# Optimization experiments

Measured on AMD Instinct MI355X. Metric: run time of the kernel, lower is better.

Reference implementation:

```python
import jax, jax.numpy as jnp
import numpy as np

V, H, B, T, L, G = 32000, 256, 16, 128, 50, 8
BETA, GAMMA = 5.0, 2.0
ATOL = 1e-8  # torch.allclose(x, zeros) default atol (rtol term vanishes vs zero)


def setup_inputs() -> dict:
    key = jax.random.key(0)
    ks = jax.random.split(key, 17)
    u = 1.0 / np.sqrt(H)
    def U(k, shape):
        return jax.random.uniform(k, shape, jnp.float32, -u, u)
    return dict(
        recipe=jax.random.randint(ks[0], (B, T), 0, V),
        g=jax.random.randint(ks[1], (B, G), 0, V),
        ingr=jax.random.randint(ks[2], (B, L), 0, V),
        wv=jax.random.normal(ks[3], (V, H), jnp.float32) * 0.1,  # frozen word vectors
        w_ih=U(ks[4], (5 * H, H)),
        w_hh=U(ks[5], (5 * H, H)),
        b_ih=U(ks[6], (5 * H,)),
        b_hh=U(ks[7], (5 * H,)),
        Z=U(ks[8], (H, H)),
        Y=U(ks[9], (H, H)),
        U_g=U(ks[10], (H, H)),
        z_bias=U(ks[11], (H,)),
        y_bias=U(ks[12], (H,)),
        S=U(ks[13], (3, H)),
        P=U(ks[14], (H, H)),
        fcW=U(ks[15], (V, H)),
        fcb=U(ks[16], (V,)),
    )


def _cgru_forward(x, g_vec, E, w_ih, w_hh, b_ih, b_hh, Z, Y, U_g, z_bias, y_bias, S, P):
    # x: (B,T,H) batch_first; g_vec: (B,H); E: (B,L,H)
    ht0 = g_vec @ U_g.T                      # init_hidden
    a0 = jnp.zeros((x.shape[0], E.shape[1]), x.dtype)
    E0 = E                                   # (1-a)*E with a=0
    ot0 = jnp.zeros_like(x[:, 0])
    goal_term = g_vec @ Y.T + y_bias         # constant across steps

    def step(carry, x_t):
        ht, ot, a, E_new = carry
        is_zero = jnp.all(jnp.abs(x_t) <= ATOL)
        # --- cell ---
        gi = x_t @ w_ih.T + b_ih
        gh = ht @ w_hh.T + b_hh
        i_r, i_u, i_n, i_g, i_i = jnp.split(gi, 5, axis=1)
        h_r, h_u, h_n, h_g, h_i = jnp.split(gh, 5, axis=1)
        z_t = jax.nn.sigmoid(i_u + h_u)
        r_t = jax.nn.sigmoid(i_r + h_r)
        s_t = jax.nn.sigmoid(i_g + h_g)
        q_t = jax.nn.sigmoid(i_i + h_i)
        tmp = E_new.sum(axis=1)              # 'mlk -> mk'
        h_tilde = jnp.tanh(i_n + r_t * h_n + s_t * goal_term + q_t * (tmp @ Z.T + z_bias))
        ht2 = h_tilde + z_t * (ht - h_tilde)
        # --- attention read/write ---
        ref = jax.nn.softmax((BETA * ht2) @ S.T, axis=-1)   # (B,3)
        h_proj = ht2 @ P.T
        En = (1.0 - a)[:, :, None] * E
        alpha_n = jax.nn.softmax(GAMMA * jnp.einsum('mk,mlk->ml', h_proj, En), axis=-1)
        c_n = jnp.einsum('mlk,ml->mk', E, alpha_n)
        Eu = a[:, :, None] * E
        alpha_u = jax.nn.softmax(GAMMA * jnp.einsum('mk,mlk->ml', h_proj, Eu), axis=-1)
        c_u = jnp.einsum('mlk,ml->mk', E, alpha_u)
        out = ref[:, 0:1] * h_proj + ref[:, 1:2] * c_n + ref[:, 2:3] * c_u
        a2 = a + ref[:, 1:2] * alpha_n
        # skip update when input step is all-zero (faithful to torch.allclose guard)
        ht_o = jnp.where(is_zero, ht, ht2)
        ot_o = jnp.where(is_zero, ot, out)
        a_o = jnp.where(is_zero, a, a2)
        E_o = jnp.where(is_zero, E_new, En)
        return (ht_o, ot_o, a_o, E_o), ot_o

    (ht, ot, a, E_new), outs = jax.lax.scan(step, (ht0, ot0, a0, E0),
                                            jnp.transpose(x, (1, 0, 2)))
    output = jnp.transpose(outs, (1, 0, 2))  # back to batch_first (B,T,H)
    return output, ht, a, E_new


def reference(recipe, g, ingr, wv, w_ih, w_hh, b_ih, b_hh, Z, Y, U_g,
              z_bias, y_bias, S, P, fcW, fcb):
    recipe_embed = wv[recipe]           # (B,T,H)
    goal_embed = wv[g].sum(axis=1)      # (B,H)
    E = wv[ingr]                        # (B,L,H)
    output, ht, a, E_new = _cgru_forward(recipe_embed, goal_embed, E,
                                         w_ih, w_hh, b_ih, b_hh, Z, Y, U_g,
                                         z_bias, y_bias, S, P)
    logits = output @ fcW.T + fcb       # (B,T,V)
    return logits, ht, a, E_new
```

## Files before the change

### kernel.cpp

```cpp
#include <hip/hip_runtime.h>

#define Hd   256
#define Bd   16
#define Td   128
#define Ld   50
#define Vd   32000
#define G5H  1280

typedef __attribute__((ext_vector_type(8))) short short8v;
typedef __attribute__((ext_vector_type(4))) float f32x4;

__device__ __forceinline__ unsigned short f2bu(float f) {
  unsigned u = __float_as_uint(f);
  unsigned r = (u + 0x7fffu + ((u >> 16) & 1u)) >> 16;
  return (unsigned short)r;
}
__device__ __forceinline__ float bu2f(unsigned short b) {
  return __uint_as_float(((unsigned)b) << 16);
}
__device__ __forceinline__ float sigm(float x) { return 1.f / (1.f + __expf(-x)); }

__device__ __forceinline__ void st_devu(unsigned* p, unsigned v) {
  __hip_atomic_store(p, v, __ATOMIC_RELAXED, __HIP_MEMORY_SCOPE_AGENT);
}
__device__ __forceinline__ unsigned ld_devu(const unsigned* p) {
  return __hip_atomic_load((unsigned*)p, __ATOMIC_RELAXED, __HIP_MEMORY_SCOPE_AGENT);
}
__device__ __forceinline__ void st_devd(double* p, double v) {
  __hip_atomic_store(p, v, __ATOMIC_RELAXED, __HIP_MEMORY_SCOPE_AGENT);
}
__device__ __forceinline__ double ld_devd(const double* p) {
  return __hip_atomic_load((double*)p, __ATOMIC_RELAXED, __HIP_MEMORY_SCOPE_AGENT);
}
__device__ __forceinline__ double pk2(float a, float b) {
  union { double d; float2 f; } u; u.f = make_float2(a, b); return u.d;
}

__global__ __launch_bounds__(256) void conv_kernel(
    const float* __restrict__ wv, const float* __restrict__ w_ih,
    const float* __restrict__ fcW, const float* __restrict__ w_hh,
    const float* __restrict__ Zm, const float* __restrict__ Pm,
    unsigned short* __restrict__ wv_b, unsigned short* __restrict__ wih_b,
    unsigned short* __restrict__ fcw_b, unsigned short* __restrict__ whh_f,
    unsigned short* __restrict__ z_f, unsigned short* __restrict__ p_f)
{
  const long N0 = 2048000, N1 = N0 + 81920, N2 = N1 + 2048000;
  const long NW = 81920, NZ = 16384, NP = 16384;
  const long N5 = N2 + NW + NZ + NP;
  for (long idx = (long)blockIdx.x * blockDim.x + threadIdx.x; idx < N5;
       idx += (long)gridDim.x * blockDim.x) {
    if (idx < N2) {
      const float* src; unsigned short* dst; long off;
      if      (idx < N0) { src = wv;   dst = wv_b;  off = idx; }
      else if (idx < N1) { src = w_ih; dst = wih_b; off = idx - N0; }
      else               { src = fcW;  dst = fcw_b; off = idx - N1; }
      float4 v = *(const float4*)(src + off * 4);
      ushort4 o;
      o.x = f2bu(v.x); o.y = f2bu(v.y); o.z = f2bu(v.z); o.w = f2bu(v.w);
      *(ushort4*)(dst + off * 4) = o;
    } else {
      long u = idx - N2;
      const float* src; unsigned short* dst;
      if      (u < NW)      { src = w_hh; dst = whh_f; }
      else if (u < NW + NZ) { src = Zm;   dst = z_f;  u -= NW; }
      else                  { src = Pm;   dst = p_f;  u -= NW + NZ; }
      long frag = u >> 7;
      int g128 = (int)(u & 127);
      int lane = g128 >> 1, e0 = (g128 & 1) * 4;
      long T = frag >> 3; int ks = (int)(frag & 7);
      int lr = lane & 15, lg = lane >> 4;
      float4 v = *(const float4*)(src + (T * 16 + lr) * 256 + ks * 32 + lg * 8 + e0);
      ushort4 o;
      o.x = f2bu(v.x); o.y = f2bu(v.y); o.z = f2bu(v.z); o.w = f2bu(v.w);
      *(ushort4*)(dst + u * 4) = o;
    }
  }
}

__global__ __launch_bounds__(256) void prep_kernel(
    const int* __restrict__ g, const int* __restrict__ ingr,
    const float* __restrict__ wv, const float* __restrict__ Ug,
    const float* __restrict__ Ym, const float* __restrict__ yb,
    float* __restrict__ E_ws, float* __restrict__ sumE,
    float* __restrict__ goal_ws, float* __restrict__ HT0)
{
  __shared__ float ge[256];
  const int b = blockIdx.x, tid = threadIdx.x;
  float s = 0.f;
  for (int i = 0; i < 8; ++i) s += wv[((size_t)g[(b << 3) + i] << 8) + tid];
  ge[tid] = s;
  __syncthreads();
  float h0 = 0.f, gt = 0.f;
  const float* ur = Ug + (tid << 8);
  const float* yr = Ym + (tid << 8);
#pragma unroll 8
  for (int k = 0; k < Hd; k += 4) {
    float4 gv = *(const float4*)(ge + k);
    float4 uv = *(const float4*)(ur + k);
    float4 yv = *(const float4*)(yr + k);
    h0 = fmaf(gv.x, uv.x, h0); h0 = fmaf(gv.y, uv.y, h0);
    h0 = fmaf(gv.z, uv.z, h0); h0 = fmaf(gv.w, uv.w, h0);
    gt = fmaf(gv.x, yv.x, gt); gt = fmaf(gv.y, yv.y, gt);
    gt = fmaf(gv.z, yv.z, gt); gt = fmaf(gv.w, yv.w, gt);
  }
  HT0[(b << 8) + tid] = h0;
  goal_ws[(b << 8) + tid] = gt + yb[tid];
  float se = 0.f;
  for (int l = 0; l < Ld; ++l) {
    float v = wv[((size_t)ingr[b * Ld + l] << 8) + tid];
    E_ws[((size_t)(b * Ld + l) << 8) + tid] = v;
    se += v;
  }
  sumE[(b << 8) + tid] = se;
}

template <int MODE>
__global__ __launch_bounds__(256) void gemm_bf16(
    const unsigned short* __restrict__ A, const unsigned short* __restrict__ Bmat,
    const int* __restrict__ ridx, const float* __restrict__ bias,
    float* __restrict__ C)
{
  __shared__ unsigned short As[128 * 64];
  __shared__ unsigned short Bs[128 * 64];
  const int tid = threadIdx.x;
  const int m0 = blockIdx.x << 7, n0 = blockIdx.y << 7;
  const int wave = tid >> 6, lane = tid & 63;
  const int wm = wave >> 1, wn = wave & 1;
  const int lr = lane & 15, lg = lane >> 4;

  f32x4 acc[4][4];
#pragma unroll
  for (int i = 0; i < 4; ++i)
#pragma unroll
    for (int jj = 0; jj < 4; ++jj) acc[i][jj] = (f32x4){0.f, 0.f, 0.f, 0.f};

  const int srow = tid >> 1, shalf = tid & 1;
  const unsigned short* arow;
  {
    int gm = m0 + srow;
    if (MODE == 0) {
      int tt = gm >> 4, bb = gm & 15;
      arow = A + (size_t)ridx[bb * Td + tt] * Hd;
    } else {
      arow = A + (size_t)gm * Hd;
    }
  }
  const unsigned short* brow = Bmat + (size_t)(n0 + srow) * Hd;

  for (int k0 = 0; k0 < Hd; k0 += 64) {
#pragma unroll
    for (int c = 0; c < 4; ++c) {
      int k = shalf * 32 + c * 8;
      uint4 va = *(const uint4*)(arow + k0 + k);
      uint4 vb = *(const uint4*)(brow + k0 + k);
      int byo = (srow << 7) + ((k << 1) ^ ((srow & 7) << 4));
      *(uint4*)((char*)As + byo) = va;
      *(uint4*)((char*)Bs + byo) = vb;
    }
    __syncthreads();
#pragma unroll
    for (int kk = 0; kk < 2; ++kk) {
      short8v af[4], bfr[4];
      const int kb = kk * 32 + lg * 8;
#pragma unroll
      for (int i = 0; i < 4; ++i) {
        int ar = wm * 64 + i * 16 + lr;
        af[i] = *(const short8v*)((const char*)As + (ar << 7) + ((kb << 1) ^ ((ar & 7) << 4)));
        int br = wn * 64 + i * 16 + lr;
        bfr[i] = *(const short8v*)((const char*)Bs + (br << 7) + ((kb << 1) ^ ((br & 7) << 4)));
      }
#pragma unroll
      for (int i = 0; i < 4; ++i)
#pragma unroll
        for (int jj = 0; jj < 4; ++jj)
          acc[i][jj] = __builtin_amdgcn_mfma_f32_16x16x32_bf16(af[i], bfr[jj], acc[i][jj], 0, 0, 0);
    }
    __syncthreads();
  }
#pragma unroll
  for (int i = 0; i < 4; ++i)
#pragma unroll
    for (int jj = 0; jj < 4; ++jj) {
      int col = n0 + wn * 64 + jj * 16 + lr;
      float bv = bias[col];
#pragma unroll
      for (int r = 0; r < 4; ++r) {
        int row = m0 + wm * 64 + i * 16 + lg * 4 + r;
        float v = acc[i][jj][r] + bv;
        if (MODE == 0) {
          int tt = row >> 4, bb = row & 15;
          C[((size_t)(bb * Td + tt)) * G5H + col] = v;
        } else {
          C[(size_t)row * Vd + col] = v;
        }
      }
    }
}

#define RNN_SMEM 150080
__global__ __launch_bounds__(512, 1) void rnn_kernel(
    const unsigned short* __restrict__ whh_f, const unsigned short* __restrict__ z_f,
    const unsigned short* __restrict__ p_f, const float* __restrict__ b_hh,
    const float* __restrict__ Sm, const float* __restrict__ z_bias,
    const float* __restrict__ gi, const float* __restrict__ goal_ws,
    const float* __restrict__ E_ws, const float* __restrict__ sumE,
    const float* __restrict__ HT0,
    unsigned short* __restrict__ out_all, float* __restrict__ d_out,
    double* __restrict__ XH, double* __restrict__ XP, unsigned* __restrict__ FL)
{
  extern __shared__ char smem[];
  unsigned short* w_lds = (unsigned short*)(smem);
  unsigned short* z_lds = (unsigned short*)(smem + 81920);
  unsigned short* p_lds = (unsigned short*)(smem + 98304);
  unsigned short* E_lds = (unsigned short*)(smem + 114688);
  float* hp    = (float*)(smem + 141088);
  float* gh_l  = (float*)(smem + 142112);
  float* zd    = (float*)(smem + 142752);
  float* se    = (float*)(smem + 142880);
  float* gl    = (float*)(smem + 143904);
  float* bh    = (float*)(smem + 144032);
  float* zb    = (float*)(smem + 144672);
  float* Sl    = (float*)(smem + 144800);
  float* a_l   = (float*)(smem + 145184);
  float* d_l   = (float*)(smem + 145440);
  float* an_l  = (float*)(smem + 145696);
  float* au_l  = (float*)(smem + 145952);
  float* sd    = (float*)(smem + 146208);
  float* refl  = (float*)(smem + 146224);
  unsigned short* tp_hi = (unsigned short*)(smem + 146240);
  unsigned short* tp_lo = (unsigned short*)(smem + 146752);
  unsigned short* hs_hi = (unsigned short*)(smem + 147264);
  unsigned short* hs_lo = (unsigned short*)(smem + 147328);
  float* hrow  = (float*)(smem + 147392);
  unsigned short* ht_hi = (unsigned short*)(smem + 148416);
  unsigned short* ht_lo = (unsigned short*)(smem + 148928);
  float* gi_l  = (float*)(smem + 149440);

  const int b  = blockIdx.x >> 3;
  const int j  = blockIdx.x & 7;
  const int hc0 = j << 5;
  const int tid = threadIdx.x;
  const int lane = tid & 63, wid = tid >> 6;
  const int lr = lane & 15, lg = lane >> 4;
  unsigned* FLb = FL + (b << 5);

  for (int idx = tid; idx < 5120; idx += 512) {
    int f = idx >> 6, e = idx & 63;
    int q = f >> 3, ks = f & 7;
    int T = (q >> 1) * 16 + 2 * j + (q & 1);
    *(uint4*)(w_lds + ((size_t)f << 9) + e * 8) =
        *(const uint4*)(whh_f + (((size_t)T * 8 + ks) << 9) + e * 8);
  }
  for (int idx = tid; idx < 1024; idx += 512) {
    int f = idx >> 6, e = idx & 63;
    int T = 2 * j + (f >> 3), ks = f & 7;
    *(uint4*)(z_lds + ((size_t)f << 9) + e * 8) =
        *(const uint4*)(z_f + (((size_t)T * 8 + ks) << 9) + e * 8);
  }
  for (int idx = tid; idx < 1024; idx += 512) {
    int f = idx >> 6, e = idx & 63;
    *(uint4*)(p_lds + ((size_t)f << 9) + e * 8) =
        *(const uint4*)(p_f + (((size_t)f * 8 + j) << 9) + e * 8);
  }
  for (int idx = tid; idx < Ld * 256; idx += 512) {
    int l = idx >> 8, k = idx & 255;
    E_lds[l * 264 + (k >> 5) * 33 + (k & 31)] =
        f2bu(E_ws[((size_t)(b * Ld + l) << 8) + k]);
  }
  if (tid < 160) bh[tid] = b_hh[((tid >> 5) << 8) + hc0 + (tid & 31)];
  if (tid < 96) Sl[tid] = Sm[((tid >> 5) << 8) + hc0 + (tid & 31)];
  if (tid < 32) {
    gl[tid] = goal_ws[(b << 8) + hc0 + tid];
    zb[tid] = z_bias[hc0 + tid];
  }
  if (tid < 256) {
    float s0 = sumE[(b << 8) + tid];
    se[tid] = s0;
    unsigned short hi = f2bu(s0);
    tp_hi[tid] = hi; tp_lo[tid] = f2bu(s0 - bu2f(hi));
    float h0 = HT0[(b << 8) + tid];
    hrow[tid] = h0;
    unsigned short hh = f2bu(h0);
    ht_hi[tid] = hh; ht_lo[tid] = f2bu(h0 - bu2f(hh));
  }
  if (tid < 64) a_l[tid] = 0.f;
  __syncthreads();

  if (wid < 4) {
#pragma unroll
    for (int i = 0; i < 3; ++i) {
      int q = wid + 4 * i;
      if (q < 10) {
        f32x4 acc = (f32x4){0.f, 0.f, 0.f, 0.f};
#pragma unroll
        for (int ks = 0; ks < 8; ++ks) {
          short8v av = *(const short8v*)(w_lds + ((size_t)(q * 8 + ks) << 9) + (lane << 3));
          short8v bv = (short8v){0,0,0,0,0,0,0,0};
          if (lr < 2)
            bv = *(const short8v*)((lr == 0 ? ht_hi : ht_lo) + ks * 32 + (lg << 3));
          acc = __builtin_amdgcn_mfma_f32_16x16x32_bf16(av, bv, acc, 0, 0, 0);
        }
#pragma unroll
        for (int r = 0; r < 4; ++r) {
          float v = acc[r] + __shfl_xor(acc[r], 1);
          if (lr == 0) gh_l[q * 16 + lg * 4 + r] = v;
        }
      }
    }
  } else if (wid == 4 || wid == 5) {
    int tz = wid - 4;
    f32x4 acc = (f32x4){0.f, 0.f, 0.f, 0.f};
#pragma unroll
    for (int ks = 0; ks < 8; ++ks) {
      short8v av = *(const short8v*)(z_lds + ((size_t)(tz * 8 + ks) << 9) + (lane << 3));
      short8v bv = (short8v){0,0,0,0,0,0,0,0};
      if (lr < 2)
        bv = *(const short8v*)((lr == 0 ? tp_hi : tp_lo) + ks * 32 + (lg << 3));
      acc = __builtin_amdgcn_mfma_f32_16x16x32_bf16(av, bv, acc, 0, 0, 0);
    }
#pragma unroll
    for (int r = 0; r < 4; ++r) {
      float v = acc[r] + __shfl_xor(acc[r], 1);
      if (lr == 0) zd[tz * 16 + lg * 4 + r] = v;
    }
  }
  __syncthreads();
  {
    double* XHp = XH + ((size_t)((0 * 16 + b) * 8 + j)) * 16;
    double* XPp = XP + ((size_t)((0 * 16 + b) * 8 + j)) * 132;
    if (tid < 32) {
      int cl = tid;
      const float* gib = gi + ((size_t)(b * Td)) * G5H + hc0 + cl;
      float g_ir = gib[0], g_iu = gib[256], g_in = gib[512];
      float g_ig = gib[768], g_ii = gib[1024];
      float hr = gh_l[cl]       + bh[cl];
      float hu = gh_l[32 + cl]  + bh[32 + cl];
      float hn = gh_l[64 + cl]  + bh[64 + cl];
      float hg = gh_l[96 + cl]  + bh[96 + cl];
      float hq = gh_l[128 + cl] + bh[128 + cl];
      float rt = sigm(g_ir + hr), zt = sigm(g_iu + hu);
      float st = sigm(g_ig + hg), qt = sigm(g_ii + hq);
      float htl = tanhf(g_in + rt * hn + st * gl[cl] + qt * (zd[cl] + zb[cl]));
      float h2 = htl + zt * (hrow[hc0 + cl] - htl);
      unsigned short hi = f2bu(h2);
      hs_hi[cl] = hi; hs_lo[cl] = f2bu(h2 - bu2f(hi));
      float h2o = __shfl_xor(h2, 1);
      if (!(cl & 1)) st_devd(XHp + (cl >> 1), pk2(h2, h2o));
      float p0 = Sl[cl] * h2, p1 = Sl[32 + cl] * h2, p2 = Sl[64 + cl] * h2;
      p0 += __shfl_xor(p0, 1);  p0 += __shfl_xor(p0, 2);  p0 += __shfl_xor(p0, 4);
      p0 += __shfl_xor(p0, 8);  p0 += __shfl_xor(p0, 16);
      p1 += __shfl_xor(p1, 1);  p1 += __shfl_xor(p1, 2);  p1 += __shfl_xor(p1, 4);
      p1 += __shfl_xor(p1, 8);  p1 += __shfl_xor(p1, 16);
      p2 += __shfl_xor(p2, 1);  p2 += __shfl_xor(p2, 2);  p2 += __shfl_xor(p2, 4);
      p2 += __shfl_xor(p2, 8);  p2 += __shfl_xor(p2, 16);
      if (cl == 0) {
        st_devd(XPp + 128, pk2(p0, p1));
        st_devd(XPp + 129, pk2(p2, 0.f));
      }
    }
    __syncthreads();
#pragma unroll
    for (int qq = 0; qq < 2; ++qq) {
      int q = wid * 2 + qq;
      short8v av = *(const short8v*)(p_lds + ((size_t)q << 9) + (lane << 3));
      short8v bv = (short8v){0,0,0,0,0,0,0,0};
      if (lr < 2)
        bv = *(const short8v*)((lr == 0 ? hs_hi : hs_lo) + (lg << 3));
      f32x4 acc = (f32x4){0.f, 0.f, 0.f, 0.f};
      acc = __builtin_amdgcn_mfma_f32_16x16x32_bf16(av, bv, acc, 0, 0, 0);
      float v0 = acc[0] + __shfl_xor(acc[0], 1);
      float v1 = acc[1] + __shfl_xor(acc[1], 1);
      float v2 = acc[2] + __shfl_xor(acc[2], 1);
      float v3 = acc[3] + __shfl_xor(acc[3], 1);
      if (lr == 0) {
        st_devd(XPp + q * 8 + lg * 2, pk2(v0, v1));
        st_devd(XPp + q * 8 + lg * 2 + 1, pk2(v2, v3));
      }
    }
    asm volatile("s_waitcnt vmcnt(0)" ::: "memory");
    __syncthreads();
    if (tid == 0) st_devu(FLb + j, 1u);
  }

  for (int t = 0; t < Td; ++t) {
    const int par = t & 1, par1 = (t + 1) & 1;
    const double* XPr = XP + ((size_t)((par * 16 + b) * 8)) * 132;
    const double* XHr = XH + ((size_t)((par * 16 + b) * 8)) * 16;
    double* XPp = XP + ((size_t)((par1 * 16 + b) * 8 + j)) * 132;
    double* XHp = XH + ((size_t)((par1 * 16 + b) * 8 + j)) * 16;
    if (tid < 256) {
      int k = tid;
      int kp = (k >> 5) * 33 + (k & 31);
      float acct = 0.f;
#pragma unroll 10
      for (int l = 0; l < Ld; ++l)
        acct = fmaf(a_l[l], bu2f(E_lds[l * 264 + kp]), acct);
      float tn = se[k] - acct;
      unsigned short th = f2bu(tn);
      tp_hi[k] = th; tp_lo[k] = f2bu(tn - bu2f(th));
    } else {
      unsigned tgt = (unsigned)(t + 1);
      int guard = 0;
      while (1) {
        unsigned v = (lane < 8) ? ld_devu(FLb + lane) : tgt;
        if (__all((int)(v >= tgt))) break;
        __builtin_amdgcn_s_sleep(1);
        if (++guard > (1 << 20)) break;
      }
      int u = tid - 256;
      if (u < 128) {
        float2 f0, f1, f2, f3, f4, f5, f6, f7;
        { union { double d; float2 f; } u_;
          u_.d = ld_devd(XPr + 0 * 132 + u); f0 = u_.f;
          u_.d = ld_devd(XPr + 1 * 132 + u); f1 = u_.f;
          u_.d = ld_devd(XPr + 2 * 132 + u); f2 = u_.f;
          u_.d = ld_devd(XPr + 3 * 132 + u); f3 = u_.f;
          u_.d = ld_devd(XPr + 4 * 132 + u); f4 = u_.f;
          u_.d = ld_devd(XPr + 5 * 132 + u); f5 = u_.f;
          u_.d = ld_devd(XPr + 6 * 132 + u); f6 = u_.f;
          u_.d = ld_devd(XPr + 7 * 132 + u); f7 = u_.f; }
        hp[2 * u] =
          ((((((f0.x + f1.x) + f2.x) + f3.x) + f4.x) + f5.x) + f6.x) + f7.x;
        hp[2 * u + 1] =
          ((((((f0.y + f1.y) + f2.y) + f3.y) + f4.y) + f5.y) + f6.y) + f7.y;
      } else if (u < 192) {
        int d0 = 2 * (u - 128);
#pragma unroll
        for (int s = 0; s < 2; ++s) {
          int d = d0 + s;
          union { double d; float2 f; } u_;
          u_.d = ld_devd(XHr + (d >> 4) * 16 + (d & 15));
          int c0 = (d >> 4) * 32 + 2 * (d & 15);
          float a0 = u_.f.x, a1 = u_.f.y;
          hrow[c0] = a0; hrow[c0 + 1] = a1;
          unsigned short h0 = f2bu(a0), h1 = f2bu(a1);
          ht_hi[c0] = h0;     ht_lo[c0] = f2bu(a0 - bu2f(h0));
          ht_hi[c0 + 1] = h1; ht_lo[c0 + 1] = f2bu(a1 - bu2f(h1));
          if (t == Td - 1 && j == 0) {
            d_out[(size_t)65536000 + (b << 8) + c0] = a0;
            d_out[(size_t)65536000 + (b << 8) + c0 + 1] = a1;
          }
        }
      } else {
        int u2 = u - 192;
        if (u2 < 3) {
          float2 f[8];
#pragma unroll
          for (int js = 0; js < 8; ++js) {
            union { double d; float2 f; } u_;
            u_.d = ld_devd(XPr + js * 132 + 128 + (u2 >> 1));
            f[js] = u_.f;
          }
          float sx, sy;
          sx = ((((((f[0].x + f[1].x) + f[2].x) + f[3].x) + f[4].x) + f[5].x)
                + f[6].x) + f[7].x;
          sy = ((((((f[0].y + f[1].y) + f[2].y) + f[3].y) + f[4].y) + f[5].y)
                + f[6].y) + f[7].y;
          sd[u2] = (u2 & 1) ? sy : ((u2 == 0) ? sx : sx);
          if (u2 == 0) { sd[0] = sx; sd[1] = sy; }
          else if (u2 == 2) sd[2] = sx;
        } else if (u2 >= 8 && u2 < 40 && t < Td - 1) {
          int c = u2 - 8;
          const float* gib = gi + ((size_t)(b * Td + t + 1)) * G5H + hc0 + c;
          gi_l[c]       = gib[0];
          gi_l[32 + c]  = gib[256];
          gi_l[64 + c]  = gib[512];
          gi_l[96 + c]  = gib[768];
          gi_l[128 + c] = gib[1024];
        }
      }
    }
    __syncthreads();
    if (wid < 2) {
      int tz = wid;
      f32x4 acc = (f32x4){0.f, 0.f, 0.f, 0.f};
#pragma unroll
      for (int ks = 0; ks < 8; ++ks) {
        short8v av = *(const short8v*)(z_lds + ((size_t)(tz * 8 + ks) << 9) + (lane << 3));
        short8v bv = (short8v){0,0,0,0,0,0,0,0};
        if (lr < 2)
          bv = *(const short8v*)((lr == 0 ? tp_hi : tp_lo) + ks * 32 + (lg << 3));
        acc = __builtin_amdgcn_mfma_f32_16x16x32_bf16(av, bv, acc, 0, 0, 0);
      }
#pragma unroll
      for (int r = 0; r < 4; ++r) {
        float v = acc[r] + __shfl_xor(acc[r], 1);
        if (lr == 0) zd[tz * 16 + lg * 4 + r] = v;
      }
    } else if (wid < 4) {
#pragma unroll
      for (int i = 0; i < 5; ++i) {
        int q = (wid - 2) * 5 + i;
        f32x4 acc = (f32x4){0.f, 0.f, 0.f, 0.f};
#pragma unroll
        for (int ks = 0; ks < 8; ++ks) {
          short8v av = *(const short8v*)(w_lds + ((size_t)(q * 8 + ks) << 9) + (lane << 3));
          short8v bv = (short8v){0,0,0,0,0,0,0,0};
          if (lr < 2)
            bv = *(const short8v*)((lr == 0 ? ht_hi : ht_lo) + ks * 32 + (lg << 3));
          acc = __builtin_amdgcn_mfma_f32_16x16x32_bf16(av, bv, acc, 0, 0, 0);
        }
#pragma unroll
        for (int r = 0; r < 4; ++r) {
          float v = acc[r] + __shfl_xor(acc[r], 1);
          if (lr == 0) gh_l[q * 16 + lg * 4 + r] = v;
        }
      }
    } else {
      int u = tid - 256;
      if (u < 200) {
        int l = u >> 2, q = u & 3;
        const unsigned short* er0 = E_lds + l * 264 + q * 66;
        const float* hq = hp + (q << 6);
        float p = 0.f;
#pragma unroll 8
        for (int i = 0; i < 16; ++i) {
          unsigned uu = *(const unsigned*)(er0 + 2 * i);
          float e0 = __uint_as_float(uu << 16);
          float e1 = __uint_as_float(uu & 0xffff0000u);
          p = fmaf(e0, hq[2 * i], p);
          p = fmaf(e1, hq[2 * i + 1], p);
        }
        const unsigned short* er1 = er0 + 33;
        const float* hq1 = hq + 32;
#pragma unroll 8
        for (int i = 0; i < 16; ++i) {
          unsigned uu = *(const unsigned*)(er1 + 2 * i);
          float e0 = __uint_as_float(uu << 16);
          float e1 = __uint_as_float(uu & 0xffff0000u);
          p = fmaf(e0, hq1[2 * i], p);
          p = fmaf(e1, hq1[2 * i + 1], p);
        }
        p += __shfl_xor(p, 1); p += __shfl_xor(p, 2);
        if (q == 0) d_l[l] = p;
      } else if (u == 204) {
        float s0 = 5.0f * sd[0], s1 = 5.0f * sd[1], s2 = 5.0f * sd[2];
        float m = fmaxf(s0, fmaxf(s1, s2));
        float e0 = __expf(s0 - m), e1 = __expf(s1 - m), e2 = __expf(s2 - m);
        float inv = 1.f / (e0 + e1 + e2);
        refl[0] = e0 * inv; refl[1] = e1 * inv; refl[2] = e2 * inv;
      }
    }
    __syncthreads();
    if (tid < 32) {
      if (t < Td - 1) {
        int cl = tid;
        float hr = gh_l[cl]       + bh[cl];
        float hu = gh_l[32 + cl]  + bh[32 + cl];
        float hn = gh_l[64 + cl]  + bh[64 + cl];
        float hg = gh_l[96 + cl]  + bh[96 + cl];
        float hq = gh_l[128 + cl] + bh[128 + cl];
        float rt = sigm(gi_l[cl] + hr), zt = sigm(gi_l[32 + cl] + hu);
        float st = sigm(gi_l[96 + cl] + hg), qt = sigm(gi_l[128 + cl] + hq);
        float htl = tanhf(gi_l[64 + cl] + rt * hn + st * gl[cl] + qt * (zd[cl] + zb[cl]));
        float h2 = htl + zt * (hrow[hc0 + cl] - htl);
        unsigned short hi = f2bu(h2);
        hs_hi[cl] = hi; hs_lo[cl] = f2bu(h2 - bu2f(hi));
        float h2o = __shfl_xor(h2, 1);
        if (!(cl & 1)) st_devd(XHp + (cl >> 1), pk2(h2, h2o));
        float p0 = Sl[cl] * h2, p1 = Sl[32 + cl] * h2, p2 = Sl[64 + cl] * h2;
        p0 += __shfl_xor(p0, 1);  p0 += __shfl_xor(p0, 2);  p0 += __shfl_xor(p0, 4);
        p0 += __shfl_xor(p0, 8);  p0 += __shfl_xor(p0, 16);
        p1 += __shfl_xor(p1, 1);  p1 += __shfl_xor(p1, 2);  p1 += __shfl_xor(p1, 4);
        p1 += __shfl_xor(p1, 8);  p1 += __shfl_xor(p1, 16);
        p2 += __shfl_xor(p2, 1);  p2 += __shfl_xor(p2, 2);  p2 += __shfl_xor(p2, 4);
        p2 += __shfl_xor(p2, 8);  p2 += __shfl_xor(p2, 16);
        if (cl == 0) {
          st_devd(XPp + 128, pk2(p0, p1));
          st_devd(XPp + 129, pk2(p2, 0.f));
        }
      }
    } else if (tid >= 64 && tid < 192) {
      int u = tid - 64;
      int which = u >> 6;
      int l = u & 63;
      float dv;
      if (which == 0) dv = (l < Ld) ? 2.0f * (1.f - a_l[l]) * d_l[l] : -3.4e38f;
      else            dv = (l < Ld) ? 2.0f * a_l[l] * d_l[l]         : -3.4e38f;
      float m = dv;
      m = fmaxf(m, __shfl_xor(m, 1));  m = fmaxf(m, __shfl_xor(m, 2));
      m = fmaxf(m, __shfl_xor(m, 4));  m = fmaxf(m, __shfl_xor(m, 8));
      m = fmaxf(m, __shfl_xor(m, 16)); m = fmaxf(m, __shfl_xor(m, 32));
      float e = (l < Ld) ? __expf(dv - m) : 0.f;
      float ss = e;
      ss += __shfl_xor(ss, 1);  ss += __shfl_xor(ss, 2);  ss += __shfl_xor(ss, 4);
      ss += __shfl_xor(ss, 8);  ss += __shfl_xor(ss, 16); ss += __shfl_xor(ss, 32);
      float al = e / ss;
      if (which == 0) an_l[l] = al; else au_l[l] = al;
    }
    __syncthreads();
    if (wid < 4) {
      if (t < Td - 1) {
#pragma unroll
        for (int qq = 0; qq < 4; ++qq) {
          int q = wid * 4 + qq;
          short8v av = *(const short8v*)(p_lds + ((size_t)q << 9) + (lane << 3));
          short8v bv = (short8v){0,0,0,0,0,0,0,0};
          if (lr < 2)
            bv = *(const short8v*)((lr == 0 ? hs_hi : hs_lo) + (lg << 3));
          f32x4 acc = (f32x4){0.f, 0.f, 0.f, 0.f};
          acc = __builtin_amdgcn_mfma_f32_16x16x32_bf16(av, bv, acc, 0, 0, 0);
          float v0 = acc[0] + __shfl_xor(acc[0], 1);
          float v1 = acc[1] + __shfl_xor(acc[1], 1);
          float v2 = acc[2] + __shfl_xor(acc[2], 1);
          float v3 = acc[3] + __shfl_xor(acc[3], 1);
          if (lr == 0) {
            st_devd(XPp + q * 8 + lg * 2, pk2(v0, v1));
            st_devd(XPp + q * 8 + lg * 2 + 1, pk2(v2, v3));
          }
        }
      }
    } else {
      int k = tid - 256;
      int kp = (k >> 5) * 33 + (k & 31);
      float accn = 0.f, accu = 0.f;
#pragma unroll 10
      for (int l = 0; l < Ld; ++l) {
        float e = bu2f(E_lds[l * 264 + kp]);
        accn = fmaf(an_l[l], e, accn);
        accu = fmaf(au_l[l], e, accu);
      }
      float outv = refl[0] * hp[k] + refl[1] * accn + refl[2] * accu;
      if ((t & 7) == j) {
        out_all[(((b << 7) + t) << 8) + k] = f2bu(outv);
        if (t == Td - 1) {
          for (int l = 0; l < Ld; ++l) {
            size_t o = ((size_t)(b * Ld + l) << 8) + k;
            d_out[(size_t)65540896 + o] = (1.f - a_l[l]) * E_ws[o];
          }
        }
      }
      if (t < Td - 1 && k < Ld)
        a_l[k] = a_l[k] + refl[1] * an_l[k];
    }
    asm volatile("s_waitcnt vmcnt(0)" ::: "memory");
    __syncthreads();
    if (t < Td - 1) {
      if (tid == 0) st_devu(FLb + j, (unsigned)(t + 2));
    } else {
      if (tid < Ld) {
        float na = a_l[tid] + refl[1] * an_l[tid];
        if (j == 7) d_out[(size_t)65540096 + b * Ld + tid] = na;
      }
    }
  }
}

extern "C" void kernel_launch(void* const* d_in, const int* in_sizes, int n_in,
                              void* d_out, int out_size, void* d_ws, size_t ws_size,
                              hipStream_t stream)
{
  const int*   recipe = (const int*)d_in[0];
  const int*   g      = (const int*)d_in[1];
  const int*   ingr   = (const int*)d_in[2];
  const float* wv     = (const float*)d_in[3];
  const float* w_ih   = (const float*)d_in[4];
  const float* w_hh   = (const float*)d_in[5];
  const float* b_ih   = (const float*)d_in[6];
  const float* b_hh   = (const float*)d_in[7];
  const float* Z      = (const float*)d_in[8];
  const float* Y      = (const float*)d_in[9];
  const float* Ug     = (const float*)d_in[10];
  const float* z_bias = (const float*)d_in[11];
  const float* y_bias = (const float*)d_in[12];
  const float* S      = (const float*)d_in[13];
  const float* P      = (const float*)d_in[14];
  const float* fcW    = (const float*)d_in[15];
  const float* fcb    = (const float*)d_in[16];
  float* out = (float*)d_out;
  char* ws = (char*)d_ws;

  size_t off = 0;
  unsigned* FL             = (unsigned*)(ws + off);        off += 2048;
  double* XH               = (double*)(ws + off);          off += 32768;
  double* XP               = (double*)(ws + off);          off += 270336;
  unsigned short* wv_b     = (unsigned short*)(ws + off);  off += 16384000;
  unsigned short* wih_b    = (unsigned short*)(ws + off);  off += 655360;
  unsigned short* fcw_b    = (unsigned short*)(ws + off);  off += 16384000;
  unsigned short* whh_f    = (unsigned short*)(ws + off);  off += 655360;
  unsigned short* z_f      = (unsigned short*)(ws + off);  off += 131072;
  unsigned short* p_f      = (unsigned short*)(ws + off);  off += 131072;
  float* gi_ws             = (float*)(ws + off);           off += 10485760;
  float* E_ws              = (float*)(ws + off);           off += 819200;
  float* sumE              = (float*)(ws + off);           off += 16384;
  float* goal_ws           = (float*)(ws + off);           off += 16384;
  float* HT0               = (float*)(ws + off);           off += 16384;
  unsigned short* out_all  = (unsigned short*)(ws + off);  off += 1048576;

  hipMemsetAsync(FL, 0, 2048, stream);
  conv_kernel<<<4096, 256, 0, stream>>>(wv, w_ih, fcW, w_hh, Z, P,
                                        wv_b, wih_b, fcw_b, whh_f, z_f, p_f);
  prep_kernel<<<16, 256, 0, stream>>>(g, ingr, wv, Ug, Y, y_bias,
                                      E_ws, sumE, goal_ws, HT0);
  gemm_bf16<0><<<dim3(16, 10), 256, 0, stream>>>(wv_b, wih_b, recipe, b_ih, gi_ws);
  hipFuncSetAttribute((const void*)rnn_kernel,
                      hipFuncAttributeMaxDynamicSharedMemorySize, RNN_SMEM);
  rnn_kernel<<<128, 512, RNN_SMEM, stream>>>(whh_f, z_f, p_f, b_hh, S, z_bias,
                                             gi_ws, goal_ws, E_ws, sumE, HT0,
                                             out_all, out, XH, XP, FL);
  gemm_bf16<1><<<dim3(16, 250), 256, 0, stream>>>(out_all, fcw_b, nullptr, fcb, out);
}
```

Baseline: 1.405 ms.

## Move P-projection into wave 0 and publish step flag before block barriers

Wave 0 now computes the new hidden slice, then runs all 16 P-projection MFMAs itself, drains its stores and publishes the step flag right away. Before, it waited for two more block barriers and shared the P work across four waves. The gh and Z matmul tiles are also rebalanced: three waves split the ten gate tiles and one wave takes both Z tiles. This shortens the cross-block critical path of the recurrence, so other blocks can begin the next step sooner. The cost is serializing the P matmul on a single wave.

```diff
diff --git a/kernel.cpp b/kernel.cpp
--- a/kernel.cpp
+++ b/kernel.cpp
@@ -456,7 +456,6 @@
                 + f[6].x) + f[7].x;
           sy = ((((((f[0].y + f[1].y) + f[2].y) + f[3].y) + f[4].y) + f[5].y)
                 + f[6].y) + f[7].y;
-          sd[u2] = (u2 & 1) ? sy : ((u2 == 0) ? sx : sx);
           if (u2 == 0) { sd[0] = sx; sd[1] = sy; }
           else if (u2 == 2) sd[2] = sx;
         } else if (u2 >= 8 && u2 < 40 && t < Td - 1) {
@@ -471,39 +470,45 @@
       }
     }
     __syncthreads();
-    if (wid < 2) {
-      int tz = wid;
-      f32x4 acc = (f32x4){0.f, 0.f, 0.f, 0.f};
-#pragma unroll
-      for (int ks = 0; ks < 8; ++ks) {
-        short8v av = *(const short8v*)(z_lds + ((size_t)(tz * 8 + ks) << 9) + (lane << 3));
-        short8v bv = (short8v){0,0,0,0,0,0,0,0};
-        if (lr < 2)
-          bv = *(const short8v*)((lr == 0 ? tp_hi : tp_lo) + ks * 32 + (lg << 3));
-        acc = __builtin_amdgcn_mfma_f32_16x16x32_bf16(av, bv, acc, 0, 0, 0);
-      }
-#pragma unroll
-      for (int r = 0; r < 4; ++r) {
-        float v = acc[r] + __shfl_xor(acc[r], 1);
-        if (lr == 0) zd[tz * 16 + lg * 4 + r] = v;
-      }
-    } else if (wid < 4) {
-#pragma unroll
-      for (int i = 0; i < 5; ++i) {
-        int q = (wid - 2) * 5 + i;
+    if (wid == 0 || wid == 2 || wid == 3) {
+      int base0 = (wid == 0) ? 0 : (wid == 2 ? 4 : 7);
+      int cnt   = (wid == 0) ? 4 : 3;
+#pragma unroll 4
+      for (int i = 0; i < 4; ++i) {
+        if (i < cnt) {
+          int q = base0 + i;
+          f32x4 acc = (f32x4){0.f, 0.f, 0.f, 0.f};
+#pragma unroll
+          for (int ks = 0; ks < 8; ++ks) {
+            short8v av = *(const short8v*)(w_lds + ((size_t)(q * 8 + ks) << 9) + (lane << 3));
+            short8v bv = (short8v){0,0,0,0,0,0,0,0};
+            if (lr < 2)
+              bv = *(const short8v*)((lr == 0 ? ht_hi : ht_lo) + ks * 32 + (lg << 3));
+            acc = __builtin_amdgcn_mfma_f32_16x16x32_bf16(av, bv, acc, 0, 0, 0);
+          }
+#pragma unroll
+          for (int r = 0; r < 4; ++r) {
+            float v = acc[r] + __shfl_xor(acc[r], 1);
+            if (lr == 0) gh_l[q * 16 + lg * 4 + r] = v;
+          }
+        }
+      }
+    } else if (wid == 1) {
+#pragma unroll
+      for (int tz = 0; tz < 2; ++tz) {
         f32x4 acc = (f32x4){0.f, 0.f, 0.f, 0.f};
 #pragma unroll
         for (int ks = 0; ks < 8; ++ks) {
-          short8v av = *(const short8v*)(w_lds + ((size_t)(q * 8 + ks) << 9) + (lane << 3));
+          short8v av = *(const short8v*)(z_lds + ((size_t)(tz * 8 + ks) << 9) + (lane << 3));
           short8v bv = (short8v){0,0,0,0,0,0,0,0};
           if (lr < 2)
-            bv = *(const short8v*)((lr == 0 ? ht_hi : ht_lo) + ks * 32 + (lg << 3));
+            bv = *(const short8v*)((lr == 0 ? tp_hi : tp_lo) + ks * 32 + (lg << 3));
           acc = __builtin_amdgcn_mfma_f32_16x16x32_bf16(av, bv, acc, 0, 0, 0);
         }
 #pragma unroll
         for (int r = 0; r < 4; ++r) {
           float v = acc[r] + __shfl_xor(acc[r], 1);
-          if (lr == 0) gh_l[q * 16 + lg * 4 + r] = v;
+          if (lr == 0) zd[tz * 16 + lg * 4 + r] = v;
         }
       }
     } else {
@@ -542,33 +547,56 @@
       }
     }
     __syncthreads();
-    if (tid < 32) {
+    if (wid == 0) {
       if (t < Td - 1) {
-        int cl = tid;
-        float hr = gh_l[cl]       + bh[cl];
-        float hu = gh_l[32 + cl]  + bh[32 + cl];
-        float hn = gh_l[64 + cl]  + bh[64 + cl];
-        float hg = gh_l[96 + cl]  + bh[96 + cl];
-        float hq = gh_l[128 + cl] + bh[128 + cl];
-        float rt = sigm(gi_l[cl] + hr), zt = sigm(gi_l[32 + cl] + hu);
-        float st = sigm(gi_l[96 + cl] + hg), qt = sigm(gi_l[128 + cl] + hq);
-        float htl = tanhf(gi_l[64 + cl] + rt * hn + st * gl[cl] + qt * (zd[cl] + zb[cl]));
-        float h2 = htl + zt * (hrow[hc0 + cl] - htl);
-        unsigned short hi = f2bu(h2);
-        hs_hi[cl] = hi; hs_lo[cl] = f2bu(h2 - bu2f(hi));
-        float h2o = __shfl_xor(h2, 1);
-        if (!(cl & 1)) st_devd(XHp + (cl >> 1), pk2(h2, h2o));
-        float p0 = Sl[cl] * h2, p1 = Sl[32 + cl] * h2, p2 = Sl[64 + cl] * h2;
-        p0 += __shfl_xor(p0, 1);  p0 += __shfl_xor(p0, 2);  p0 += __shfl_xor(p0, 4);
-        p0 += __shfl_xor(p0, 8);  p0 += __shfl_xor(p0, 16);
-        p1 += __shfl_xor(p1, 1);  p1 += __shfl_xor(p1, 2);  p1 += __shfl_xor(p1, 4);
-        p1 += __shfl_xor(p1, 8);  p1 += __shfl_xor(p1, 16);
-        p2 += __shfl_xor(p2, 1);  p2 += __shfl_xor(p2, 2);  p2 += __shfl_xor(p2, 4);
-        p2 += __shfl_xor(p2, 8);  p2 += __shfl_xor(p2, 16);
-        if (cl == 0) {
-          st_devd(XPp + 128, pk2(p0, p1));
-          st_devd(XPp + 129, pk2(p2, 0.f));
-        }
+        if (lane < 32) {
+          int cl = lane;
+          float hr = gh_l[cl]       + bh[cl];
+          float hu = gh_l[32 + cl]  + bh[32 + cl];
+          float hn = gh_l[64 + cl]  + bh[64 + cl];
+          float hg = gh_l[96 + cl]  + bh[96 + cl];
+          float hq = gh_l[128 + cl] + bh[128 + cl];
+          float rt = sigm(gi_l[cl] + hr), zt = sigm(gi_l[32 + cl] + hu);
+          float st = sigm(gi_l[96 + cl] + hg), qt = sigm(gi_l[128 + cl] + hq);
+          float htl = tanhf(gi_l[64 + cl] + rt * hn + st * gl[cl] + qt * (zd[cl] + zb[cl]));
+          float h2 = htl + zt * (hrow[hc0 + cl] - htl);
+          unsigned short hi = f2bu(h2);
+          hs_hi[cl] = hi; hs_lo[cl] = f2bu(h2 - bu2f(hi));
+          float h2o = __shfl_xor(h2, 1);
+          if (!(cl & 1)) st_devd(XHp + (cl >> 1), pk2(h2, h2o));
+          float p0 = Sl[cl] * h2, p1 = Sl[32 + cl] * h2, p2 = Sl[64 + cl] * h2;
+          p0 += __shfl_xor(p0, 1);  p0 += __shfl_xor(p0, 2);  p0 += __shfl_xor(p0, 4);
+          p0 += __shfl_xor(p0, 8);  p0 += __shfl_xor(p0, 16);
+          p1 += __shfl_xor(p1, 1);  p1 += __shfl_xor(p1, 2);  p1 += __shfl_xor(p1, 4);
+          p1 += __shfl_xor(p1, 8);  p1 += __shfl_xor(p1, 16);
+          p2 += __shfl_xor(p2, 1);  p2 += __shfl_xor(p2, 2);  p2 += __shfl_xor(p2, 4);
+          p2 += __shfl_xor(p2, 8);  p2 += __shfl_xor(p2, 16);
+          if (cl == 0) {
+            st_devd(XPp + 128, pk2(p0, p1));
+            st_devd(XPp + 129, pk2(p2, 0.f));
+          }
+        }
+        asm volatile("s_waitcnt lgkmcnt(0)" ::: "memory");
+        __builtin_amdgcn_sched_barrier(0);
+#pragma unroll
+        for (int q = 0; q < 16; ++q) {
+          short8v av = *(const short8v*)(p_lds + ((size_t)q << 9) + (lane << 3));
+          short8v bv = (short8v){0,0,0,0,0,0,0,0};
+          if (lr < 2)
+            bv = *(const short8v*)((lr == 0 ? hs_hi : hs_lo) + (lg << 3));
+          f32x4 acc = (f32x4){0.f, 0.f, 0.f, 0.f};
+          acc = __builtin_amdgcn_mfma_f32_16x16x32_bf16(av, bv, acc, 0, 0, 0);
+          float v0 = acc[0] + __shfl_xor(acc[0], 1);
+          float v1 = acc[1] + __shfl_xor(acc[1], 1);
+          float v2 = acc[2] + __shfl_xor(acc[2], 1);
+          float v3 = acc[3] + __shfl_xor(acc[3], 1);
+          if (lr == 0) {
+            st_devd(XPp + q * 8 + lg * 2, pk2(v0, v1));
+            st_devd(XPp + q * 8 + lg * 2 + 1, pk2(v2, v3));
+          }
+        }
+        asm volatile("s_waitcnt vmcnt(0)" ::: "memory");
+        if (tid == 0) st_devu(FLb + j, (unsigned)(t + 2));
       }
     } else if (tid >= 64 && tid < 192) {
       int u = tid - 64;
@@ -589,28 +617,7 @@
       if (which == 0) an_l[l] = al; else au_l[l] = al;
     }
     __syncthreads();
-    if (wid < 4) {
-      if (t < Td - 1) {
-#pragma unroll
-        for (int qq = 0; qq < 4; ++qq) {
-          int q = wid * 4 + qq;
-          short8v av = *(const short8v*)(p_lds + ((size_t)q << 9) + (lane << 3));
-          short8v bv = (short8v){0,0,0,0,0,0,0,0};
-          if (lr < 2)
-            bv = *(const short8v*)((lr == 0 ? hs_hi : hs_lo) + (lg << 3));
-          f32x4 acc = (f32x4){0.f, 0.f, 0.f, 0.f};
-          acc = __builtin_amdgcn_mfma_f32_16x16x32_bf16(av, bv, acc, 0, 0, 0);
-          float v0 = acc[0] + __shfl_xor(acc[0], 1);
-          float v1 = acc[1] + __shfl_xor(acc[1], 1);
-          float v2 = acc[2] + __shfl_xor(acc[2], 1);
-          float v3 = acc[3] + __shfl_xor(acc[3], 1);
-          if (lr == 0) {
-            st_devd(XPp + q * 8 + lg * 2, pk2(v0, v1));
-            st_devd(XPp + q * 8 + lg * 2 + 1, pk2(v2, v3));
-          }
-        }
-      }
-    } else {
+    if (tid >= 256) {
       int k = tid - 256;
       int kp = (k >> 5) * 33 + (k & 31);
       float accn = 0.f, accu = 0.f;
@@ -633,15 +640,10 @@
       if (t < Td - 1 && k < Ld)
         a_l[k] = a_l[k] + refl[1] * an_l[k];
     }
-    asm volatile("s_waitcnt vmcnt(0)" ::: "memory");
     __syncthreads();
-    if (t < Td - 1) {
-      if (tid == 0) st_devu(FLb + j, (unsigned)(t + 2));
-    } else {
-      if (tid < Ld) {
-        float na = a_l[tid] + refl[1] * an_l[tid];
-        if (j == 7) d_out[(size_t)65540096 + b * Ld + tid] = na;
-      }
+    if (t == Td - 1 && tid < Ld) {
+      float na = a_l[tid] + refl[1] * an_l[tid];
+      if (j == 7) d_out[(size_t)65540096 + b * Ld + tid] = na;
     }
   }
 }
```

New measurement: 1.678 ms. 19.4% more time.
